# Kernel tuning notes

Hardware: AMD Instinct MI355X
Metric: run time of the kernel (lower is better)

Reference implementation:

```python
import jax, jax.numpy as jnp
import numpy as np

N, F_IN, H, E, G, L, T = 50000, 64, 256, 800000, 2048, 4, 4
EPS = 1e-5


def setup_inputs() -> dict:
    key = jax.random.key(0)
    ks = jax.random.split(key, 20)
    x = jax.random.normal(ks[0], (N, F_IN), dtype=jnp.float32)
    edge_index = jax.random.randint(ks[1], (2, E), 0, N, dtype=jnp.int64)
    batch = jnp.sort(jax.random.randint(ks[2], (N,), 0, G, dtype=jnp.int64))
    s = 0.05
    return {
        "x": x,
        "edge_index": edge_index,
        "batch": batch,
        "proj_W": jax.random.normal(ks[3], (F_IN, H), dtype=jnp.float32) * s,
        "proj_b": jnp.zeros((H,), dtype=jnp.float32),
        "conv_W": jax.random.normal(ks[4], (L, H, H), dtype=jnp.float32) * s,
        "conv_b": jnp.zeros((L, H), dtype=jnp.float32),
        "bn_gamma": jnp.ones((L, H), dtype=jnp.float32),
        "bn_beta": jnp.zeros((L, H), dtype=jnp.float32),
        "bn_mean": jax.random.normal(ks[5], (L, H), dtype=jnp.float32) * 0.1,
        "bn_var": jax.random.uniform(ks[6], (L, H), dtype=jnp.float32) * 0.5 + 0.75,
        "head_W1": jax.random.normal(ks[7], (2 * H, H), dtype=jnp.float32) * s,
        "head_b1": jnp.zeros((H,), dtype=jnp.float32),
        "head_W2": jax.random.normal(ks[8], (H, H // 2), dtype=jnp.float32) * s,
        "head_b2": jnp.zeros((H // 2,), dtype=jnp.float32),
        "head_W3": jax.random.normal(ks[9], (H // 2, T), dtype=jnp.float32) * s,
        "head_b3": jnp.zeros((T,), dtype=jnp.float32),
    }


def _gcn_conv(h, W, b, src, dst, inv_sqrt_deg):
    # PyG GCNConv: symmetric normalization with self-loops
    hW = h @ W  # [N, H]
    norm = inv_sqrt_deg[src] * inv_sqrt_deg[dst]  # [E]
    msgs = hW[src] * norm[:, None]  # [E, H] edge messages
    agg = jax.ops.segment_sum(msgs, dst, num_segments=N)
    agg = agg + hW * (inv_sqrt_deg ** 2)[:, None]  # self-loop term
    return agg + b


def reference(x, edge_index, batch, proj_W, proj_b, conv_W, conv_b,
              bn_gamma, bn_beta, bn_mean, bn_var,
              head_W1, head_b1, head_W2, head_b2, head_W3, head_b3):
    src, dst = edge_index[0], edge_index[1]
    # degree with self-loops
    deg = jax.ops.segment_sum(jnp.ones((E,), x.dtype), dst, num_segments=N) + 1.0
    inv_sqrt_deg = jax.lax.rsqrt(deg)

    h = jax.nn.relu(x @ proj_W + proj_b)
    for i in range(L):
        res = h
        h = _gcn_conv(h, conv_W[i], conv_b[i], src, dst, inv_sqrt_deg)
        # BatchNorm (eval mode: running stats); dropout inactive in eval
        h = (h - bn_mean[i]) * jax.lax.rsqrt(bn_var[i] + EPS) * bn_gamma[i] + bn_beta[i]
        h = jax.nn.relu(h)
        h = h + res

    counts = jax.ops.segment_sum(jnp.ones((N,), x.dtype), batch, num_segments=G)
    x_mean = jax.ops.segment_sum(h, batch, num_segments=G) / jnp.maximum(counts, 1.0)[:, None]
    x_max = jax.ops.segment_max(h, batch, num_segments=G)
    g = jnp.concatenate([x_mean, x_max], axis=1)  # [G, 2H]

    g = jax.nn.relu(g @ head_W1 + head_b1)
    g = jax.nn.relu(g @ head_W2 + head_b2)
    return g @ head_W3 + head_b3  # [G, T]
```

## Files before the change

kernel.cpp:

```cpp
#include <hip/hip_runtime.h>
#include <hip/hip_bf16.h>
#include <hip/hip_fp16.h>

#define N_NODES 50000
#define F_IN    64
#define HDIM    256
#define E_EDGES 800000
#define G_GRAPHS 2048
#define L_LAYERS 4
#define T_OUT   4
#define BN_EPS  1e-5f

#define NPAD    50176
#define SLICES  4
#define DMAX    48
#define NGRP    8
#define NR_GRP  6250
#define ECHUNK  2000

#define WT_CONV 0
#define WT_PROJ 262144
#define WT_H1   278528
#define WT_H2   409600
#define WT_TOT  442368

typedef _Float16 half8 __attribute__((ext_vector_type(8)));
typedef float    f32x4 __attribute__((ext_vector_type(4)));
typedef __attribute__((address_space(1))) const void gvoid;
typedef __attribute__((address_space(3))) void lvoid;


__global__ void k_deg_wcvt(const int* __restrict__ src, const int* __restrict__ dst,
                           int* __restrict__ cnt, ushort* __restrict__ pcsr,
                           const float* __restrict__ convW, const float* __restrict__ projW,
                           const float* __restrict__ W1, const float* __restrict__ W2,
                           _Float16* __restrict__ Wt,
                           const float* __restrict__ convb, const float* __restrict__ gamma,
                           const float* __restrict__ beta, const float* __restrict__ mean,
                           const float* __restrict__ var, float* __restrict__ bnp,
                           ushort* __restrict__ Wh) {
    int grp = blockIdx.x & (NGRP - 1);
    int chunk = blockIdx.x >> 3;
    int ebase = chunk * ECHUNK;
    int lo = grp * NR_GRP;
    for (int e = ebase + threadIdx.x; e < ebase + ECHUNK; e += 256) {
        int d = dst[e];
        if ((unsigned)(d - lo) < (unsigned)NR_GRP) {
            int pos = atomicAdd(&cnt[d], 1);
            if (pos < DMAX) pcsr[(size_t)d * DMAX + pos] = (ushort)src[e];
        }
    }

    int i = blockIdx.x * 256 + threadIdx.x;
    if (i < 262144) {
        int l = i >> 16, r = i & 65535;
        int k = r >> 8, n = r & 255;
        int off = ((n >> 4) * 8 + (k >> 5)) * 512 + (n & 15) * 32 + ((k >> 3) & 3) * 8 + (k & 7);
        Wt[WT_CONV + (size_t)l * 65536 + off] = (_Float16)convW[(size_t)l * 65536 + k * 256 + n];
        return;
    }
    int j = i - 262144;
    if (j >= 0 && j < 16384) {
        int k = j >> 8, n = j & 255;
        int off = ((n >> 4) * 2 + (k >> 5)) * 512 + (n & 15) * 32 + ((k >> 3) & 3) * 8 + (k & 7);
        Wt[WT_PROJ + off] = (_Float16)projW[k * 256 + n];
        return;
    }
    j -= 16384;
    if (j >= 0 && j < 131072) {
        int k = j >> 8, n = j & 255;
        int off = ((n >> 4) * 16 + (k >> 5)) * 512 + (n & 15) * 32 + ((k >> 3) & 3) * 8 + (k & 7);
        Wt[WT_H1 + off] = (_Float16)W1[k * 256 + n];
        return;
    }
    j -= 131072;
    if (j >= 0 && j < 32768) {
        int k = j >> 7, n = j & 127;
        int off = ((n >> 4) * 8 + (k >> 5)) * 512 + (n & 15) * 32 + ((k >> 3) & 3) * 8 + (k & 7);
        Wt[WT_H2 + off] = (_Float16)W2[k * 128 + n];
        return;
    }
    j -= 32768;
    if (j >= 0 && j < L_LAYERS * HDIM) {
        float scv = gamma[j] * rsqrtf(var[j] + BN_EPS);
        bnp[j] = scv;
        bnp[L_LAYERS * HDIM + j] = (convb[j] - mean[j]) * scv + beta[j];
        return;
    }
    j -= L_LAYERS * HDIM;
    if (j >= 0 && j < SLICES * 64) {
        int sl = j >> 6, w = j & 63;
        Wh[((size_t)sl * NPAD + N_NODES) * 64 + w] = 0;
    }
}

__global__ __launch_bounds__(256) void k_proj_mfma(const float* __restrict__ x,
                                                   const _Float16* __restrict__ Wpt,
                                                   const float* __restrict__ bias,
                                                   ushort* __restrict__ h16, int nrows) {
    __shared__ _Float16 hs[64 * 264];
    int block_r = blockIdx.x * 64;
#pragma unroll
    for (int ii = 0; ii < 4; ii++) {
        int i = threadIdx.x + 256 * ii;
        int row = i >> 4;
        int c4 = (i & 15) * 4;
        float4 v = (block_r + row < nrows)
                       ? *(const float4*)(x + (size_t)(block_r + row) * F_IN + c4)
                       : make_float4(0.f, 0.f, 0.f, 0.f);
        _Float16* p = &hs[row * 72 + c4];
        p[0] = (_Float16)v.x; p[1] = (_Float16)v.y;
        p[2] = (_Float16)v.z; p[3] = (_Float16)v.w;
    }
    __syncthreads();

    int wave = threadIdx.x >> 6;
    int lane = threadIdx.x & 63;
    int l16 = lane & 15;
    int quad = lane >> 4;
    int n0 = wave * 64;
    int loff = l16 * 32 + quad * 8;

    f32x4 acc[4][4] = {};
#pragma unroll
    for (int k0 = 0; k0 < F_IN; k0 += 32) {
        half8 a[4], b[4];
#pragma unroll
        for (int ai = 0; ai < 4; ai++)
            a[ai] = *(const half8*)&hs[(ai * 16 + l16) * 72 + k0 + quad * 8];
#pragma unroll
        for (int bj = 0; bj < 4; bj++)
            b[bj] = *(const half8*)&Wpt[(size_t)(((wave * 4 + bj) * 2 + (k0 >> 5)) * 512) + loff];
#pragma unroll
        for (int ai = 0; ai < 4; ai++)
#pragma unroll
            for (int bj = 0; bj < 4; bj++)
                acc[ai][bj] = __builtin_amdgcn_mfma_f32_16x16x32_f16(a[ai], b[bj], acc[ai][bj], 0, 0, 0);
    }
    __syncthreads();

#pragma unroll
    for (int ai = 0; ai < 4; ai++) {
#pragma unroll
        for (int r = 0; r < 4; r++) {
            int lrow = ai * 16 + quad * 4 + r;
#pragma unroll
            for (int bj = 0; bj < 4; bj++) {
                int col = n0 + bj * 16 + l16;
                float v = fmaxf(acc[ai][bj][r] + bias[col], 0.f);
                hs[lrow * 264 + col] = (_Float16)v;
            }
        }
    }
    __syncthreads();

#pragma unroll
    for (int ii = 0; ii < 8; ii++) {
        int i = threadIdx.x + 256 * ii;
        int s = i >> 9;
        int j = i & 511;
        int lrow = j >> 3;
        int q = j & 7;
        if (block_r + lrow < nrows)
            *(uint4*)(h16 + ((size_t)s * NPAD + block_r + lrow) * 64 + q * 8) =
                *(const uint4*)&hs[lrow * 264 + s * 64 + q * 8];
    }
}

__global__ __launch_bounds__(512) void k_gemm_mfma(const ushort* __restrict__ h16,
                                                   const _Float16* __restrict__ Wt,
                                                   const int* __restrict__ cnt,
                                                   _Float16* __restrict__ outh, int nrows) {
    __shared__ _Float16 hs[2 * 128 * 128];
    int block_r = blockIdx.x * 128;
    int lane = threadIdx.x & 63;
    int wv = threadIdx.x >> 6;
    char* lds_b = (char*)hs;
    int l15 = lane & 15;
    int rsub = lane >> 4;
    int sl_lo = l15 >> 3;
    int qg = l15 & 7;

#pragma unroll
    for (int ii = 0; ii < 4; ii++) {
        int b = wv * 4 + ii;
        int row = 4 * b + rsub;
        const ushort* src = h16 + ((size_t)sl_lo * NPAD + block_r + row) * 64 + qg * 8;
        __builtin_amdgcn_global_load_lds((gvoid*)src,
                                         (lvoid*)(lds_b + b * 1024 + lane * 16), 16, 0, 0);
    }
    __syncthreads();

#pragma unroll
    for (int ii = 0; ii < 4; ii++) {
        int b = wv * 4 + ii;
        int row = 4 * b + rsub;
        const ushort* src = h16 + ((size_t)(2 + sl_lo) * NPAD + block_r + row) * 64 + qg * 8;
        __builtin_amdgcn_global_load_lds((gvoid*)src,
                                         (lvoid*)(lds_b + 32768 + b * 1024 + lane * 16), 16, 0, 0);
    }

    int wr = wv >> 2;
    int wc = wv & 3;
    int l16 = lane & 15;
    int quad = lane >> 4;
    int n0 = wc * 64;
    int r0 = wr * 64;
    int loff = l16 * 32 + quad * 8;

    f32x4 acc[4][4] = {};
#pragma unroll
    for (int kh = 0; kh < 4; kh++) {
        half8 a[4], b[4];
#pragma unroll
        for (int ai = 0; ai < 4; ai++)
            a[ai] = *(const half8*)&hs[(r0 + ai * 16 + l16) * 128 + kh * 32 + quad * 8];
#pragma unroll
        for (int bj = 0; bj < 4; bj++)
            b[bj] = *(const half8*)&Wt[(size_t)(((wc * 4 + bj) * 8 + kh) * 512) + loff];
#pragma unroll
        for (int ai = 0; ai < 4; ai++)
#pragma unroll
            for (int bj = 0; bj < 4; bj++)
                acc[ai][bj] = __builtin_amdgcn_mfma_f32_16x16x32_f16(a[ai], b[bj], acc[ai][bj], 0, 0, 0);
    }
    __syncthreads();

#pragma unroll
    for (int kh = 4; kh < 8; kh++) {
        half8 a[4], b[4];
#pragma unroll
        for (int ai = 0; ai < 4; ai++)
            a[ai] = *(const half8*)&hs[16384 + (r0 + ai * 16 + l16) * 128 + (kh - 4) * 32 + quad * 8];
#pragma unroll
        for (int bj = 0; bj < 4; bj++)
            b[bj] = *(const half8*)&Wt[(size_t)(((wc * 4 + bj) * 8 + kh) * 512) + loff];
#pragma unroll
        for (int ai = 0; ai < 4; ai++)
#pragma unroll
            for (int bj = 0; bj < 4; bj++)
                acc[ai][bj] = __builtin_amdgcn_mfma_f32_16x16x32_f16(a[ai], b[bj], acc[ai][bj], 0, 0, 0);
    }
    __syncthreads();

#pragma unroll
    for (int ai = 0; ai < 4; ai++) {
#pragma unroll
        for (int r = 0; r < 4; r++) {
            int lrow = r0 + ai * 16 + quad * 4 + r;
            float sc = rsqrtf((float)cnt[block_r + lrow] + 1.0f);
#pragma unroll
            for (int bj = 0; bj < 4; bj++) {
                int col = n0 + bj * 16 + l16;
                hs[lrow * 256 + col] = (_Float16)(acc[ai][bj][r] * sc);
            }
        }
    }
    __syncthreads();

#pragma unroll
    for (int ii = 0; ii < 8; ii++) {
        int i = threadIdx.x + 512 * ii;
        int s = i >> 10;
        int j = i & 1023;
        int lrow = j >> 3;
        int q = j & 7;
        if (block_r + lrow < nrows)
            *(uint4*)((ushort*)outh + ((size_t)s * NPAD + block_r + lrow) * 64 + q * 8) =
                *(const uint4*)&hs[lrow * 256 + s * 64 + q * 8];
    }
}

__global__ __launch_bounds__(256) void k_aggr(const int* __restrict__ cnt,
                                              const ushort* __restrict__ pcsr,
                                              const ushort* __restrict__ hWh,
                                              const float* __restrict__ bnscale,
                                              const float* __restrict__ bnshift,
                                              ushort* __restrict__ h16) {
    int slice = blockIdx.x & 3;
    int chunk = blockIdx.x >> 2;
    int lane = threadIdx.x & 63;
    int wv = threadIdx.x >> 6;
    int nb = lane >> 5;
    int g  = (lane >> 3) & 3;
    int f  = lane & 7;
    int l31 = lane & 31;
    int node = chunk * 8 + wv * 2 + nb;

    const uint4* tbl = (const uint4*)hWh + (size_t)slice * (NPAD * 8);
    const unsigned* tbl_w = (const unsigned*)tbl;
    const unsigned* h16_w = (const unsigned*)h16 + (size_t)slice * (NPAD * 32);

    int mraw = cnt[node];
    int m = (mraw > DMAX) ? DMAX : mraw;
    const ushort* crow = pcsr + (size_t)node * DMAX;

    int idx0 = (l31      < m) ? (int)crow[l31     ] : N_NODES;
    int idx1 = (l31 + 32 < m) ? (int)crow[l31 + 32] : N_NODES;

    unsigned eoff = (unsigned)node * 32u + (unsigned)(f * 4 + g);
    unsigned self_u = tbl_w[eoff];
    unsigned res_u  = __builtin_nontemporal_load(&h16_w[eoff]);
    float iv = rsqrtf((float)mraw + 1.0f);

    int mm = m;
    mm = max(mm, __shfl_xor(mm, 32));

    __half2 a0 = __floats2half2_rn(0.f, 0.f), a1 = a0, a2 = a0, a3 = a0;

#define AGGR_CHUNK(IDX, BASE)                                               \
    {                                                                       \
        _Pragma("unroll")                                                   \
        for (int jj = 0; jj < 16; jj += 4) {                                \
            int s = __shfl((IDX), (lane & 32) | ((BASE) + jj + g));         \
            uint4 u = tbl[s * 8 + f];                                       \
            const __half2* p = (const __half2*)&u;                          \
            a0 = __hadd2(a0, p[0]);                                         \
            a1 = __hadd2(a1, p[1]);                                         \
            a2 = __hadd2(a2, p[2]);                                         \
            a3 = __hadd2(a3, p[3]);                                         \
        }                                                                   \
    }

    AGGR_CHUNK(idx0, 0);
    if (mm > 16) AGGR_CHUNK(idx0, 16);
    if (mm > 32) AGGR_CHUNK(idx1, 0);
#undef AGGR_CHUNK

    __half2 accv[4] = {a0, a1, a2, a3};
#pragma unroll
    for (int i = 0; i < 4; i++) {
        unsigned pk = *(unsigned*)&accv[i];
        int q = __shfl_xor((int)pk, 8);
        accv[i] = __hadd2(accv[i], *(__half2*)&q);
        pk = *(unsigned*)&accv[i];
        q = __shfl_xor((int)pk, 16);
        accv[i] = __hadd2(accv[i], *(__half2*)&q);
    }

    unsigned A0 = *(unsigned*)&accv[0], A1 = *(unsigned*)&accv[1];
    unsigned A2 = *(unsigned*)&accv[2], A3 = *(unsigned*)&accv[3];
    unsigned v01 = (g & 1) ? A1 : A0;
    unsigned v23 = (g & 1) ? A3 : A2;
    unsigned Asel = (g & 2) ? v23 : v01;

    float2 acc2 = __half22float2(*(__half2*)&Asel);
    float2 slf2 = __half22float2(*(__half2*)&self_u);
    float2 res2 = __half22float2(*(__half2*)&res_u);
    int c0f = slice * 64 + f * 8 + g * 2;
    float2 scl = *(const float2*)(bnscale + c0f);
    float2 shf = *(const float2*)(bnshift + c0f);
    float r0 = fmaxf(fmaf((acc2.x + slf2.x) * iv, scl.x, shf.x), 0.f) + res2.x;
    float r1 = fmaxf(fmaf((acc2.y + slf2.y) * iv, scl.y, shf.y), 0.f) + res2.y;
    __half2 qo = __floats2half2_rn(r0, r1);
    __builtin_nontemporal_store(*(unsigned*)&qo, (unsigned*)&h16_w[eoff]);
}

__global__ __launch_bounds__(256) void k_pool(const ushort* __restrict__ h16,
                                              const int* __restrict__ batch,
                                              ushort* __restrict__ gp16) {
    int g = blockIdx.x;
    __shared__ int s_lo, s_hi;
    __shared__ float sm_sum[4][256];
    __shared__ float sm_max[4][256];
    if (threadIdx.x == 0) {
        int lo = 0, hi = N_NODES;
        while (lo < hi) { int m = (lo + hi) >> 1; if (batch[m] < g) lo = m + 1; else hi = m; }
        s_lo = lo;
        hi = N_NODES;
        while (lo < hi) { int m = (lo + hi) >> 1; if (batch[m] < g + 1) lo = m + 1; else hi = m; }
        s_hi = lo;
    }
    __syncthreads();
    int lo = s_lo, hi = s_hi;
    int t = threadIdx.x;
    int ng = t >> 5;
    int cg = t & 31;
    const ushort* base = h16 + ((size_t)(cg >> 3) * NPAD) * 64 + (cg & 7) * 8;

    float s8[8], m8[8];
#pragma unroll
    for (int i = 0; i < 8; i++) { s8[i] = 0.f; m8[i] = -1e30f; }
    for (int n = lo + ng; n < hi; n += 8) {
        uint4 v = *(const uint4*)(base + (size_t)n * 64);
        const __half2* p = (const __half2*)&v;
#pragma unroll
        for (int i = 0; i < 4; i++) {
            float2 fv = __half22float2(p[i]);
            s8[2 * i]     += fv.x;
            s8[2 * i + 1] += fv.y;
            m8[2 * i]     = fmaxf(m8[2 * i], fv.x);
            m8[2 * i + 1] = fmaxf(m8[2 * i + 1], fv.y);
        }
    }
#pragma unroll
    for (int i = 0; i < 8; i++) {
        s8[i] += __shfl_xor(s8[i], 32);
        m8[i] = fmaxf(m8[i], __shfl_xor(m8[i], 32));
    }
    int wv = t >> 6;
    if ((t & 32) == 0) {
#pragma unroll
        for (int i = 0; i < 8; i++) {
            sm_sum[wv][cg * 8 + i] = s8[i];
            sm_max[wv][cg * 8 + i] = m8[i];
        }
    }
    __syncthreads();
    float fs = sm_sum[0][t] + sm_sum[1][t] + sm_sum[2][t] + sm_sum[3][t];
    float fm = fmaxf(fmaxf(sm_max[0][t], sm_max[1][t]), fmaxf(sm_max[2][t], sm_max[3][t]));
    float cntf = fmaxf((float)(hi - lo), 1.0f);
    float mean = fs / cntf;
    float mxo = (hi > lo) ? fm : 0.0f;
    gp16[(size_t)g * 2 * HDIM + t] = __half_as_ushort(__float2half(mean));
    gp16[(size_t)g * 2 * HDIM + HDIM + t] = __half_as_ushort(__float2half(mxo));
}

__global__ __launch_bounds__(256) void k_head1_mfma(const ushort* __restrict__ A,
                                                    const _Float16* __restrict__ Bt,
                                                    const float* __restrict__ bias,
                                                    ushort* __restrict__ out16) {
    constexpr int K = 512, LDKH = 520;
    __shared__ _Float16 hs[64 * LDKH];
    int block_r = blockIdx.x * 64;
#pragma unroll
    for (int ii = 0; ii < 16; ii++) {
        int i = threadIdx.x + 256 * ii;
        int row = i / (K / 8);
        int c = (i % (K / 8)) * 8;
        *(uint4*)&hs[row * LDKH + c] = *(const uint4*)(A + (size_t)(block_r + row) * K + c);
    }
    __syncthreads();

    int wave = threadIdx.x >> 6;
    int lane = threadIdx.x & 63;
    int l16 = lane & 15;
    int quad = lane >> 4;
    int n0 = wave * 64;
    int loff = l16 * 32 + quad * 8;

    f32x4 acc[4][4] = {};
#pragma unroll
    for (int k0 = 0; k0 < K; k0 += 32) {
        half8 a[4], b[4];
#pragma unroll
        for (int ai = 0; ai < 4; ai++)
            a[ai] = *(const half8*)&hs[(ai * 16 + l16) * LDKH + k0 + quad * 8];
#pragma unroll
        for (int bj = 0; bj < 4; bj++)
            b[bj] = *(const half8*)&Bt[(size_t)(((wave * 4 + bj) * 16 + (k0 >> 5)) * 512) + loff];
#pragma unroll
        for (int ai = 0; ai < 4; ai++)
#pragma unroll
            for (int bj = 0; bj < 4; bj++)
                acc[ai][bj] = __builtin_amdgcn_mfma_f32_16x16x32_f16(a[ai], b[bj], acc[ai][bj], 0, 0, 0);
    }

#pragma unroll
    for (int ai = 0; ai < 4; ai++) {
        int rowb = block_r + ai * 16 + quad * 4;
#pragma unroll
        for (int r = 0; r < 4; r++) {
            int row = rowb + r;
#pragma unroll
            for (int bj = 0; bj < 4; bj++) {
                int col = n0 + bj * 16 + l16;
                float v = fmaxf(acc[ai][bj][r] + bias[col], 0.f);
                out16[(size_t)row * HDIM + col] = __half_as_ushort(__float2half(v));
            }
        }
    }
}

__global__ __launch_bounds__(128) void k_head23(const ushort* __restrict__ g1h,
                                                const _Float16* __restrict__ W2t,
                                                const float* __restrict__ b2,
                                                const float* __restrict__ W3,
                                                const float* __restrict__ b3,
                                                float* __restrict__ out) {
    __shared__ _Float16 hs[64 * 264];
    __shared__ float g2s[64 * 132];
    int block_r = blockIdx.x * 64;
#pragma unroll
    for (int ii = 0; ii < 16; ii++) {
        int i = threadIdx.x + 128 * ii;
        int row = i >> 5;
        int c = (i & 31) * 8;
        *(uint4*)&hs[row * 264 + c] = *(const uint4*)(g1h + (size_t)(block_r + row) * HDIM + c);
    }
    __syncthreads();

    int wave = threadIdx.x >> 6;
    int lane = threadIdx.x & 63;
    int l16 = lane & 15;
    int quad = lane >> 4;
    int n0 = wave * 64;
    int loff = l16 * 32 + quad * 8;

    f32x4 acc[4][4] = {};
#pragma unroll
    for (int k0 = 0; k0 < HDIM; k0 += 32) {
        half8 a[4], b[4];
#pragma unroll
        for (int ai = 0; ai < 4; ai++)
            a[ai] = *(const half8*)&hs[(ai * 16 + l16) * 264 + k0 + quad * 8];
#pragma unroll
        for (int bj = 0; bj < 4; bj++)
            b[bj] = *(const half8*)&W2t[(size_t)(((wave * 4 + bj) * 8 + (k0 >> 5)) * 512) + loff];
#pragma unroll
        for (int ai = 0; ai < 4; ai++)
#pragma unroll
            for (int bj = 0; bj < 4; bj++)
                acc[ai][bj] = __builtin_amdgcn_mfma_f32_16x16x32_f16(a[ai], b[bj], acc[ai][bj], 0, 0, 0);
    }
#pragma unroll
    for (int ai = 0; ai < 4; ai++) {
        int rowb = ai * 16 + quad * 4;
#pragma unroll
        for (int r = 0; r < 4; r++) {
            int row = rowb + r;
#pragma unroll
            for (int bj = 0; bj < 4; bj++) {
                int col = n0 + bj * 16 + l16;
                g2s[row * 132 + col] = fmaxf(acc[ai][bj][r] + b2[col], 0.f);
            }
        }
    }
    __syncthreads();

    int r = threadIdx.x >> 1;
    int p = threadIdx.x & 1;
    float a0 = b3[2 * p], a1 = b3[2 * p + 1];
#pragma unroll 8
    for (int k = 0; k < 128; k++) {
        float v = g2s[r * 132 + k];
        a0 += v * W3[k * T_OUT + 2 * p];
        a1 += v * W3[k * T_OUT + 2 * p + 1];
    }
    out[(size_t)(block_r + r) * T_OUT + 2 * p] = a0;
    out[(size_t)(block_r + r) * T_OUT + 2 * p + 1] = a1;
}

extern "C" void kernel_launch(void* const* d_in, const int* in_sizes, int n_in,
                              void* d_out, int out_size, void* d_ws, size_t ws_size,
                              hipStream_t stream) {
    const float* x     = (const float*)d_in[0];
    const int*   ei    = (const int*)d_in[1];
    const int*   batch = (const int*)d_in[2];
    const float* projW = (const float*)d_in[3];
    const float* projb = (const float*)d_in[4];
    const float* convW = (const float*)d_in[5];
    const float* convb = (const float*)d_in[6];
    const float* gamma = (const float*)d_in[7];
    const float* beta  = (const float*)d_in[8];
    const float* mean  = (const float*)d_in[9];
    const float* var   = (const float*)d_in[10];
    const float* W1    = (const float*)d_in[11];
    const float* b1    = (const float*)d_in[12];
    const float* W2    = (const float*)d_in[13];
    const float* b2    = (const float*)d_in[14];
    const float* W3    = (const float*)d_in[15];
    const float* b3    = (const float*)d_in[16];
    float* out = (float*)d_out;

    int*    cnt    = (int*)d_ws;
    ushort* pcsr   = (ushort*)(cnt + NPAD);
    ushort* hWh    = pcsr + (size_t)NPAD * DMAX;
    ushort* h16    = hWh + (size_t)NPAD * 256;
    ushort* gp16   = h16 + (size_t)NPAD * 256;
    ushort* g1h    = gp16 + (size_t)G_GRAPHS * 512;
    _Float16* Wt   = (_Float16*)(g1h + (size_t)G_GRAPHS * HDIM);
    float*  bnp    = (float*)(Wt + WT_TOT);

    hipMemsetAsync(cnt, 0, NPAD * sizeof(int), stream);
    k_deg_wcvt<<<(E_EDGES / ECHUNK) * NGRP, 256, 0, stream>>>(ei, ei + E_EDGES, cnt, pcsr,
                                                              convW, projW, W1, W2, Wt,
                                                              convb, gamma, beta, mean, var, bnp,
                                                              hWh);

    k_proj_mfma<<<(N_NODES + 63) / 64, 256, 0, stream>>>(x, Wt + WT_PROJ, projb, h16, N_NODES);

    int gemm_blocks = (N_NODES + 127) / 128;
    for (int l = 0; l < L_LAYERS; l++) {
        k_gemm_mfma<<<gemm_blocks, 512, 0, stream>>>(h16, Wt + WT_CONV + (size_t)l * HDIM * HDIM,
                                                     cnt, (_Float16*)hWh, N_NODES);
        k_aggr<<<(N_NODES / 8) * SLICES, 256, 0, stream>>>(cnt, pcsr, hWh,
                                                           bnp + l * HDIM,
                                                           bnp + L_LAYERS * HDIM + l * HDIM, h16);
    }

    k_pool<<<G_GRAPHS, HDIM, 0, stream>>>(h16, batch, gp16);
    k_head1_mfma<<<G_GRAPHS / 64, 256, 0, stream>>>(gp16, Wt + WT_H1, b1, g1h);
    k_head23<<<G_GRAPHS / 64, 128, 0, stream>>>(g1h, Wt + WT_H2, b2, W3, b3, out);
}
```

Measured before the change: 437.9 us.

## Halve GEMM LDS footprint with double-buffered K-slice staging and split epilogue

The MFMA GEMM kernel now stages the 128x256 input tile in four 64-column slices, double-buffered in 32KB of LDS instead of 64KB. Each next slice's load is issued before computing on the current one. The epilogue writes output in two 64-row halves through the smaller buffer. The aim is to halve LDS per block so more blocks fit per CU and to overlap loads with MFMA work, at the cost of extra barriers in the loop and epilogue.

After: 440.8 us. About the same (+0.6%).

```diff
diff --git a/kernel.cpp b/kernel.cpp
--- a/kernel.cpp
+++ b/kernel.cpp
@@ -171,34 +171,28 @@
                                                    const _Float16* __restrict__ Wt,
                                                    const int* __restrict__ cnt,
                                                    _Float16* __restrict__ outh, int nrows) {
-    __shared__ _Float16 hs[2 * 128 * 128];
+    __shared__ _Float16 hs[16384];
     int block_r = blockIdx.x * 128;
-    int lane = threadIdx.x & 63;
-    int wv = threadIdx.x >> 6;
+    int t = threadIdx.x;
+    int lane = t & 63;
+    int wv = t >> 6;
     char* lds_b = (char*)hs;
-    int l15 = lane & 15;
-    int rsub = lane >> 4;
-    int sl_lo = l15 >> 3;
-    int qg = l15 & 7;
-
-#pragma unroll
-    for (int ii = 0; ii < 4; ii++) {
-        int b = wv * 4 + ii;
-        int row = 4 * b + rsub;
-        const ushort* src = h16 + ((size_t)sl_lo * NPAD + block_r + row) * 64 + qg * 8;
-        __builtin_amdgcn_global_load_lds((gvoid*)src,
-                                         (lvoid*)(lds_b + b * 1024 + lane * 16), 16, 0, 0);
-    }
-    __syncthreads();
-
-#pragma unroll
-    for (int ii = 0; ii < 4; ii++) {
-        int b = wv * 4 + ii;
-        int row = 4 * b + rsub;
-        const ushort* src = h16 + ((size_t)(2 + sl_lo) * NPAD + block_r + row) * 64 + qg * 8;
-        __builtin_amdgcn_global_load_lds((gvoid*)src,
-                                         (lvoid*)(lds_b + 32768 + b * 1024 + lane * 16), 16, 0, 0);
-    }
+
+#define STAGE(C, BUF)                                                          \
+    {                                                                          \
+        _Pragma("unroll")                                                      \
+        for (int ii = 0; ii < 2; ii++) {                                       \
+            int idx = t + 512 * ii;                               \
+            int row = idx >> 3;                                                \
+            int q = idx & 7;                                                   \
+            const ushort* srcp = h16 + ((size_t)(C) * NPAD + block_r + row) * 64 + q * 8; \
+            __builtin_amdgcn_global_load_lds((gvoid*)srcp,                     \
+                (lvoid*)(lds_b + (BUF) * 16384 + idx * 16), 16, 0, 0);         \
+        }                                                                      \
+    }
+
+    STAGE(0, 0);
+    __syncthreads();
 
     int wr = wv >> 2;
     int wc = wv & 3;
@@ -210,64 +204,59 @@
 
     f32x4 acc[4][4] = {};
 #pragma unroll
-    for (int kh = 0; kh < 4; kh++) {
-        half8 a[4], b[4];
-#pragma unroll
-        for (int ai = 0; ai < 4; ai++)
-            a[ai] = *(const half8*)&hs[(r0 + ai * 16 + l16) * 128 + kh * 32 + quad * 8];
-#pragma unroll
-        for (int bj = 0; bj < 4; bj++)
-            b[bj] = *(const half8*)&Wt[(size_t)(((wc * 4 + bj) * 8 + kh) * 512) + loff];
-#pragma unroll
-        for (int ai = 0; ai < 4; ai++)
+    for (int c = 0; c < 4; c++) {
+        if (c < 3) STAGE(c + 1, (c + 1) & 1);
+        int bufo = (c & 1) * 8192;
+#pragma unroll
+        for (int kk = 0; kk < 2; kk++) {
+            half8 a[4], b[4];
+#pragma unroll
+            for (int ai = 0; ai < 4; ai++)
+                a[ai] = *(const half8*)&hs[bufo + (r0 + ai * 16 + l16) * 64 + kk * 32 + quad * 8];
 #pragma unroll
             for (int bj = 0; bj < 4; bj++)
-                acc[ai][bj] = __builtin_amdgcn_mfma_f32_16x16x32_f16(a[ai], b[bj], acc[ai][bj], 0, 0, 0);
-    }
-    __syncthreads();
-
-#pragma unroll
-    for (int kh = 4; kh < 8; kh++) {
-        half8 a[4], b[4];
-#pragma unroll
-        for (int ai = 0; ai < 4; ai++)
-            a[ai] = *(const half8*)&hs[16384 + (r0 + ai * 16 + l16) * 128 + (kh - 4) * 32 + quad * 8];
-#pragma unroll
-        for (int bj = 0; bj < 4; bj++)
-            b[bj] = *(const half8*)&Wt[(size_t)(((wc * 4 + bj) * 8 + kh) * 512) + loff];
-#pragma unroll
-        for (int ai = 0; ai < 4; ai++)
-#pragma unroll
-            for (int bj = 0; bj < 4; bj++)
-                acc[ai][bj] = __builtin_amdgcn_mfma_f32_16x16x32_f16(a[ai], b[bj], acc[ai][bj], 0, 0, 0);
-    }
-    __syncthreads();
-
-#pragma unroll
-    for (int ai = 0; ai < 4; ai++) {
-#pragma unroll
-        for (int r = 0; r < 4; r++) {
-            int lrow = r0 + ai * 16 + quad * 4 + r;
-            float sc = rsqrtf((float)cnt[block_r + lrow] + 1.0f);
-#pragma unroll
-            for (int bj = 0; bj < 4; bj++) {
-                int col = n0 + bj * 16 + l16;
-                hs[lrow * 256 + col] = (_Float16)(acc[ai][bj][r] * sc);
+                b[bj] = *(const half8*)&Wt[(size_t)(((wc * 4 + bj) * 8 + 2 * c + kk) * 512) + loff];
+#pragma unroll
+            for (int ai = 0; ai < 4; ai++)
+#pragma unroll
+                for (int bj = 0; bj < 4; bj++)
+                    acc[ai][bj] = __builtin_amdgcn_mfma_f32_16x16x32_f16(a[ai], b[bj], acc[ai][bj], 0, 0, 0);
+        }
+        __syncthreads();
+    }
+#undef STAGE
+
+#pragma unroll
+    for (int wrg = 0; wrg < 2; wrg++) {
+        if (wr == wrg) {
+#pragma unroll
+            for (int ai = 0; ai < 4; ai++) {
+#pragma unroll
+                for (int r = 0; r < 4; r++) {
+                    int lrow = ai * 16 + quad * 4 + r;
+                    float sc = rsqrtf((float)cnt[block_r + wrg * 64 + lrow] + 1.0f);
+#pragma unroll
+                    for (int bj = 0; bj < 4; bj++) {
+                        int col = n0 + bj * 16 + l16;
+                        hs[lrow * 256 + col] = (_Float16)(acc[ai][bj][r] * sc);
+                    }
+                }
             }
         }
-    }
-    __syncthreads();
-
-#pragma unroll
-    for (int ii = 0; ii < 8; ii++) {
-        int i = threadIdx.x + 512 * ii;
-        int s = i >> 10;
-        int j = i & 1023;
-        int lrow = j >> 3;
-        int q = j & 7;
-        if (block_r + lrow < nrows)
-            *(uint4*)((ushort*)outh + ((size_t)s * NPAD + block_r + lrow) * 64 + q * 8) =
-                *(const uint4*)&hs[lrow * 256 + s * 64 + q * 8];
+        __syncthreads();
+#pragma unroll
+        for (int ii = 0; ii < 4; ii++) {
+            int i = t + 512 * ii;
+            int s = i >> 9;
+            int j = i & 511;
+            int lrow = j >> 3;
+            int q = j & 7;
+            int grow = block_r + wrg * 64 + lrow;
+            if (grow < nrows)
+                *(uint4*)((ushort*)outh + ((size_t)s * NPAD + grow) * 64 + q * 8) =
+                    *(const uint4*)&hs[lrow * 256 + s * 64 + q * 8];
+        }
+        if (wrg == 0) __syncthreads();
     }
 }
 
```
